# Performance work log

Hardware: AMD Instinct MI355X
Metric: run time of the kernel (lower is better)

Reference implementation:

```python
import jax, jax.numpy as jnp
import numpy as np

D_MODEL = 1024
NUM_HEADS = 16
D_FF = 4096
SEQ = 2048
BATCH = 2
THETA = 10000.0
EPS = 1e-5


def _param(key, shape, fan_in, fan_out):
    std = 2.0 / (fan_in + fan_out) ** 0.5
    return std * jax.random.truncated_normal(key, -3.0, 3.0, shape, dtype=jnp.float32)


def setup_inputs() -> dict:
    key = jax.random.key(0)
    ks = jax.random.split(key, 8)
    d, h, f = D_MODEL, NUM_HEADS, D_FF
    return {
        'x': jax.random.normal(ks[0], (BATCH, SEQ, d), dtype=jnp.float32),
        'token_positions': jnp.arange(SEQ, dtype=jnp.int32),
        'wq': _param(ks[1], (d, d), d, d),
        'wk': _param(ks[2], (d, d), d, d),
        'wv': _param(ks[3], (d, d), d, d),
        'wo': _param(ks[4], (d, d), d, d),
        'ln1_w': jnp.ones((d,), jnp.float32),
        'ln2_w': jnp.ones((d,), jnp.float32),
        'w1': _param(ks[5], (f, d), d, f),
        'w2': _param(ks[6], (d, f), f, d),
        'w3': _param(ks[7], (f, d), d, f),
    }


def rmsnorm(x, w):
    x32 = x.astype(jnp.float32)
    rms = jnp.sqrt(jnp.mean(x32 * x32, axis=-1, keepdims=True) + EPS)
    return ((x32 / rms) * w).astype(x.dtype)


def apply_rope(x, cos, sin):
    # x: [b, h, s, d_k]; cos/sin: [s, d_k//2] -> broadcast as [1,1,s,d_k//2]
    xe, xo = x[..., ::2], x[..., 1::2]
    c = cos[None, None, :, :]
    s = sin[None, None, :, :]
    re = xe * c - xo * s
    ro = xe * s + xo * c
    return jnp.stack((re, ro), axis=-1).reshape(x.shape)


def block_forward(x, token_positions, wq, wk, wv, wo, ln1_w, ln2_w, w1, w2, w3):
    b, s, d = x.shape
    h = NUM_HEADS
    dk = d // h
    # RoPE tables at token positions
    inv_freq = 1.0 / (THETA ** (jnp.arange(0, dk // 2, dtype=jnp.float32) * 2.0 / dk))
    freqs = token_positions.astype(jnp.float32)[:, None] * inv_freq[None, :]  # [s, dk/2]
    cos, sin = jnp.cos(freqs), jnp.sin(freqs)

    # --- attention sublayer (pre-norm) ---
    xn = rmsnorm(x, ln1_w)
    q = jnp.einsum('bsd,ed->bse', xn, wq).reshape(b, s, h, dk).transpose(0, 2, 1, 3)
    k = jnp.einsum('bsd,ed->bse', xn, wk).reshape(b, s, h, dk).transpose(0, 2, 1, 3)
    v = jnp.einsum('bsd,ed->bse', xn, wv).reshape(b, s, h, dk).transpose(0, 2, 1, 3)
    q = apply_rope(q, cos, sin)
    k = apply_rope(k, cos, sin)
    scores = jnp.einsum('bhqd,bhkd->bhqk', q, k) / jnp.sqrt(jnp.float32(dk))
    causal = jnp.tril(jnp.ones((s, s), dtype=bool))
    scores = jnp.where(causal[None, None], scores, -jnp.inf)
    attn = jax.nn.softmax(scores, axis=-1)
    o = jnp.einsum('bhqk,bhkd->bhqd', attn, v)
    o = o.transpose(0, 2, 1, 3).reshape(b, s, d)
    x = x + jnp.einsum('bse,de->bsd', o, wo)

    # --- SwiGLU sublayer (pre-norm) ---
    xn = rmsnorm(x, ln2_w)
    x1 = jnp.einsum('bsd,fd->bsf', xn, w1)
    x3 = jnp.einsum('bsd,fd->bsf', xn, w3)
    gated = (x1 * jax.nn.sigmoid(x1)) * x3
    return x + jnp.einsum('bsf,df->bsd', gated, w2)


def reference(x, token_positions, wq, wk, wv, wo, ln1_w, ln2_w, w1, w2, w3):
    return block_forward(x, token_positions, wq, wk, wv, wo, ln1_w, ln2_w, w1, w2, w3)
```

## Files before the change

### kernel.cpp

```cpp
#include <hip/hip_runtime.h>
#include <hip/hip_bf16.h>

typedef __attribute__((ext_vector_type(4))) float f32x4;
typedef __attribute__((ext_vector_type(8))) short bf16x8;
typedef unsigned short u16;
typedef unsigned int u32;
typedef __attribute__((ext_vector_type(4))) u16 u16x4;

#define DEV static __device__ __forceinline__

constexpr int Bb = 2, Ss = 2048, Dd = 1024, Hh = 16, DKk = 64;
constexpr int Mm = Bb * Ss;

DEV float bf2f(u16 u) { union { u32 i; float f; } v; v.i = (u32)u << 16; return v.f; }
DEV u16 f2bf(float f) {
  union { float f; u32 i; } v; v.f = f;
  u32 r = v.i + 0x7FFFu + ((v.i >> 16) & 1u);
  return (u16)(r >> 16);
}

DEV void gload_lds16(const u16* g, u16* l) {
  __builtin_amdgcn_global_load_lds((const __attribute__((address_space(1))) u32*)g,
                                   (__attribute__((address_space(3))) u32*)l, 16, 0, 0);
}

DEV int swz16(int o) {
  return o ^ (((o >> 8) & 1) << 6) ^ (((o >> 9) & 1) << 5);
}

__global__ void k_cvt_all(const float* __restrict__ wq, const float* __restrict__ wk,
                          const float* __restrict__ wv, const float* __restrict__ wo,
                          const float* __restrict__ w1, const float* __restrict__ w2,
                          const float* __restrict__ w3,
                          u16* __restrict__ wqkv, u16* __restrict__ wob,
                          u16* __restrict__ w13, u16* __restrict__ w2b) {
  int i = (blockIdx.x * 256 + threadIdx.x) * 4;
  int seg = i >> 20;
  const float* src; u16* dst;
  if (seg == 0)      { src = wq + i;             dst = wqkv + i; }
  else if (seg == 1) { src = wk + (i - (1<<20)); dst = wqkv + i; }
  else if (seg == 2) { src = wv + (i - (2<<20)); dst = wqkv + i; }
  else if (seg == 3) { src = wo + (i - (3<<20)); dst = wob  + (i - (3<<20)); }
  else if (seg < 8)  { src = w1 + (i - (4<<20)); dst = w13  + (i - (4<<20)); }
  else if (seg < 12) { src = w2 + (i - (8<<20)); dst = w2b  + (i - (8<<20)); }
  else               { src = w3 + (i - (12<<20)); dst = w13 + (4<<20) + (i - (12<<20)); }
  float4 v = *(const float4*)src;
  u16x4 o = { f2bf(v.x), f2bf(v.y), f2bf(v.z), f2bf(v.w) };
  *(u16x4*)dst = o;
}

__global__ __launch_bounds__(256) void k_rmsnorm(const float* __restrict__ x,
                                                 const float* __restrict__ w,
                                                 u16* __restrict__ out) {
  int row = blockIdx.x;
  int t = threadIdx.x;
  float4 v = ((const float4*)(x + (long)row * Dd))[t];
  float ss = v.x * v.x + v.y * v.y + v.z * v.z + v.w * v.w;
#pragma unroll
  for (int m = 32; m; m >>= 1) ss += __shfl_xor(ss, m, 64);
  __shared__ float red[4];
  if ((t & 63) == 0) red[t >> 6] = ss;
  __syncthreads();
  float tot = red[0] + red[1] + red[2] + red[3];
  float r = rsqrtf(tot * (1.0f / Dd) + 1e-5f);
  float4 wv = ((const float4*)w)[t];
  u16x4 o = { f2bf(v.x * r * wv.x), f2bf(v.y * r * wv.y),
              f2bf(v.z * r * wv.z), f2bf(v.w * r * wv.w) };
  ((u16x4*)(out + (long)row * Dd))[t] = o;
}

__global__ void k_rope(u16* __restrict__ q, u16* __restrict__ k, const int* __restrict__ tp) {
  int idx = blockIdx.x * 256 + threadIdx.x;
  if (idx >= Bb * Ss * Hh * 32) return;
  int p = idx & 31;
  int h = (idx >> 5) & 15;
  int row = idx >> 9;
  int s = row & (Ss - 1);
  float pos = (float)tp[s];
  float invf = __expf(-(float)p * (2.0f / DKk) * 9.2103403719761836f);
  float fr = pos * invf;
  float sn, cs;
  sincosf(fr, &sn, &cs);
  long base = (long)row * Dd + h * DKk + 2 * p;
  float xe = bf2f(q[base]), xo = bf2f(q[base + 1]);
  q[base]     = f2bf((xe * cs - xo * sn) * 0.125f);
  q[base + 1] = f2bf((xe * sn + xo * cs) * 0.125f);
  xe = bf2f(k[base]); xo = bf2f(k[base + 1]);
  k[base]     = f2bf(xe * cs - xo * sn);
  k[base + 1] = f2bf(xe * sn + xo * cs);
}

__global__ void k_gate(u16* __restrict__ x1, const u16* __restrict__ x3, int n) {
  int i = (blockIdx.x * 256 + threadIdx.x) * 4;
  if (i >= n) return;
  u16x4 a = *(u16x4*)(x1 + i);
  u16x4 b = *(const u16x4*)(x3 + i);
#pragma unroll
  for (int j = 0; j < 4; j++) {
    float v = bf2f(a[j]);
    float g = v / (1.0f + __expf(-v)) * bf2f(b[j]);
    a[j] = f2bf(g);
  }
  *(u16x4*)(x1 + i) = a;
}

template <int OM, bool RES>
__global__ __launch_bounds__(256) void k_gemm(const u16* __restrict__ A,
                                              const u16* __restrict__ Bm,
                                              void* __restrict__ Cout,
                                              const float* __restrict__ Rres,
                                              int N, int K) {
  __shared__ u16 Abuf[128 * 32];
  __shared__ u16 Bbuf[128 * 32];
  const int tid = threadIdx.x;
  const int wid = tid >> 6, lane = tid & 63;
  const int wm = wid >> 1, wn = wid & 1;
  const int lq = lane >> 4, ll = lane & 15;
  const int m0 = blockIdx.y * 128, n0 = blockIdx.x * 128;

  f32x4 acc[4][4] = {};

  const int srow = tid >> 2;
  const int scol = (tid & 3) * 8;
  const long aoff = (long)(m0 + srow) * K + scol;
  const long boff = (long)(n0 + srow) * K + scol;
  u16* aldsw = Abuf + wid * 512;
  u16* bldsw = Bbuf + wid * 512;

  for (int k0 = 0; k0 < K; k0 += 32) {
    __syncthreads();
    gload_lds16(A + aoff + k0, aldsw);
    gload_lds16(A + aoff + (long)64 * K + k0, aldsw + 2048);
    gload_lds16(Bm + boff + k0, bldsw);
    gload_lds16(Bm + boff + (long)64 * K + k0, bldsw + 2048);
    __syncthreads();
    bf16x8 af[4], bfr[4];
#pragma unroll
    for (int i = 0; i < 4; i++)
      af[i] = *(const bf16x8*)&Abuf[(wm * 64 + i * 16 + ll) * 32 + lq * 8];
#pragma unroll
    for (int j = 0; j < 4; j++)
      bfr[j] = *(const bf16x8*)&Bbuf[(wn * 64 + j * 16 + ll) * 32 + lq * 8];
#pragma unroll
    for (int i = 0; i < 4; i++)
#pragma unroll
      for (int j = 0; j < 4; j++)
        acc[i][j] = __builtin_amdgcn_mfma_f32_16x16x32_bf16(af[i], bfr[j], acc[i][j], 0, 0, 0);
  }

#pragma unroll
  for (int i = 0; i < 4; i++) {
    const int rowb = m0 + wm * 64 + i * 16 + lq * 4;
#pragma unroll
    for (int j = 0; j < 4; j++) {
      const int col = n0 + wn * 64 + j * 16 + ll;
#pragma unroll
      for (int r = 0; r < 4; r++) {
        int rr = rowb + r;
        float v = acc[i][j][r];
        if (RES) v += Rres[(long)rr * N + col];
        if (OM == 1) {
          ((float*)Cout)[(long)rr * N + col] = v;
        } else {
          ((u16*)Cout)[(long)rr * N + col] = f2bf(v);
        }
      }
    }
  }
}

#define STG_A(d, h, kt)                                                         \
  { gload_lds16(A + aoff[0] + (long)(h) * 128 * K + (kt) * 64, &sA[d][h][dst0]); \
    gload_lds16(A + aoff[1] + (long)(h) * 128 * K + (kt) * 64, &sA[d][h][dst1]); }
#define STG_B(d, h, kt)                                                         \
  { gload_lds16(Bm + boff[0] + (long)(h) * 128 * K + (kt) * 64, &sB[d][h][dst0]); \
    gload_lds16(Bm + boff[1] + (long)(h) * 128 * K + (kt) * 64, &sB[d][h][dst1]); }

#define PHASE(q, d, DOB, WVN, ...)                                              \
  {                                                                             \
    bf16x8 af_[2][2];                                                           \
    _Pragma("unroll") for (int s_ = 0; s_ < 2; s_++)                            \
    _Pragma("unroll") for (int kk_ = 0; kk_ < 2; kk_++) {                       \
      int ms_ = (q) * 4 + wm * 2 + s_;                                          \
      int lo_ = ((ms_ & 7) * 16 + ll) * 128 + kk_ * 64 + lq * 16;               \
      af_[s_][kk_] = *(const bf16x8*)((const char*)sA[d][ms_ >> 3] + swz16(lo_)); \
    }                                                                           \
    if (DOB) {                                                                  \
      _Pragma("unroll") for (int ns_ = 0; ns_ < 4; ns_++)                       \
      _Pragma("unroll") for (int kk_ = 0; kk_ < 2; kk_++) {                     \
        int rl_ = wn * 64 + ns_ * 16 + ll;                                      \
        int lo_ = (rl_ & 127) * 128 + kk_ * 64 + lq * 16;                       \
        bfr[ns_][kk_] = *(const bf16x8*)((const char*)sB[d][rl_ >> 7] + swz16(lo_)); \
      }                                                                         \
    }                                                                           \
    __VA_ARGS__;                                                                \
    __builtin_amdgcn_s_barrier();                                               \
    asm volatile("s_waitcnt lgkmcnt(0)" ::: "memory");                          \
    __builtin_amdgcn_sched_barrier(0);                                          \
    __builtin_amdgcn_s_setprio(1);                                              \
    _Pragma("unroll") for (int s_ = 0; s_ < 2; s_++)                            \
    _Pragma("unroll") for (int ns_ = 0; ns_ < 4; ns_++)                         \
    _Pragma("unroll") for (int kk_ = 0; kk_ < 2; kk_++)                         \
      acc[q][s_][ns_] = __builtin_amdgcn_mfma_f32_16x16x32_bf16(                \
          af_[s_][kk_], bfr[ns_][kk_], acc[q][s_][ns_], 0, 0, 0);               \
    __builtin_amdgcn_s_setprio(0);                                              \
    { int wv_ = (WVN);                                                          \
      if (wv_ == 6) { asm volatile("s_waitcnt vmcnt(6)" ::: "memory"); }        \
      else if (wv_ == 0) { asm volatile("s_waitcnt vmcnt(0)" ::: "memory"); } } \
    __builtin_amdgcn_s_barrier();                                               \
  }

template <int OM>
__global__ __launch_bounds__(512) void k_gemm8(const u16* __restrict__ A,
                                               const u16* __restrict__ Bm,
                                               void* __restrict__ Cout,
                                               int N, int K) {
  __shared__ u16 sA[2][2][8192];
  __shared__ u16 sB[2][2][8192];
  const int nwg = gridDim.x * gridDim.y;
  const int lin = blockIdx.y * gridDim.x + blockIdx.x;
  const int swb = (lin & 7) * (nwg >> 3) + (lin >> 3);
  const int bx = swb % gridDim.x, by = swb / gridDim.x;
  const long m0 = (long)by * 256, n0 = (long)bx * 256;
  const int tid = threadIdx.x;
  const int wid = tid >> 6, lane = tid & 63;
  const int wm = wid >> 2, wn = wid & 3;
  const int lq = lane >> 4, ll = lane & 15;

  long aoff[2], boff[2];
#pragma unroll
  for (int j = 0; j < 2; j++) {
    int off = j * 8192 + wid * 1024 + lane * 16;
    int lo = swz16(off);
    int r = lo >> 7, c = (lo & 127) >> 1;
    aoff[j] = (m0 + r) * K + c;
    boff[j] = (n0 + r) * K + c;
  }
  const int dst0 = wid * 512;
  const int dst1 = 4096 + wid * 512;

  f32x4 acc[4][2][4] = {};
  bf16x8 bfr[4][2];

  const int NT = K >> 6;
  const int NI = NT >> 1;

  STG_A(0, 0, 0); STG_A(0, 1, 0); STG_B(0, 0, 0); STG_B(0, 1, 0);
  STG_B(1, 0, 1); STG_B(1, 1, 1); STG_A(1, 0, 1);
  asm volatile("s_waitcnt vmcnt(6)" ::: "memory");
  __builtin_amdgcn_s_barrier();

  for (int it = 0; it < NI; it++) {
    const int t = 2 * it;
    const bool full = (t + 2 < NT);
    PHASE(0, 0, true,  -1,            STG_A(1, 1, t + 1))
    PHASE(1, 0, false, -1,            if (full) STG_B(0, 0, t + 2))
    PHASE(2, 0, false, -1,            if (full) STG_B(0, 1, t + 2))
    PHASE(3, 0, false, full ? 6 : 0,  if (full) STG_A(0, 0, t + 2))
    PHASE(0, 1, true,  -1,            if (full) STG_A(0, 1, t + 2))
    PHASE(1, 1, false, -1,            if (full) STG_B(1, 0, t + 3))
    PHASE(2, 1, false, -1,            if (full) STG_B(1, 1, t + 3))
    PHASE(3, 1, false, full ? 6 : -1, if (full) STG_A(1, 0, t + 3))
  }

#pragma unroll
  for (int q = 0; q < 4; q++)
#pragma unroll
    for (int s = 0; s < 2; s++) {
      const long row0 = m0 + (q * 4 + wm * 2 + s) * 16 + lq * 4;
#pragma unroll
      for (int ns = 0; ns < 4; ns++) {
        const long col = n0 + wn * 64 + ns * 16 + ll;
#pragma unroll
        for (int r = 0; r < 4; r++) {
          float v = acc[q][s][ns][r];
          long rr = row0 + r;
          if (OM == 3) {
            if (col < 2048) {
              ((u16*)Cout)[(col >> 10) * (long)(Mm * 1024) + rr * 1024 + (col & 1023)] = f2bf(v);
            } else {
              int d = col & 63, hh = ((int)col >> 6) & 15;
              int b2 = (int)rr >> 11, s2 = (int)rr & (Ss - 1);
              ((u16*)Cout)[(long)(2 * Mm * 1024) + ((long)((b2 * Hh + hh) * DKk + d)) * Ss + s2] = f2bf(v);
            }
          } else {
            ((u16*)Cout)[(col >> 12) * ((long)Mm * 4096) + rr * 4096 + (col & 4095)] = f2bf(v);
          }
        }
      }
    }
}

constexpr int PPAD = 80;

DEV void attn_tile(const u16* __restrict__ Kc, const u16* __restrict__ Vc,
                   u16* __restrict__ myP, const bf16x8* qf, f32x4* accO,
                   float* mrow, float* lrow, int qloc, bool diag, int lq, int ll) {
  f32x4 sacc[4] = {};
#pragma unroll
  for (int fn = 0; fn < 4; fn++)
#pragma unroll
    for (int ks = 0; ks < 2; ks++) {
      bf16x8 kf = *(const bf16x8*)&Kc[(fn * 16 + ll) * 64 + (((ks * 4 + lq) ^ (ll & 7)) * 8)];
      sacc[fn] = __builtin_amdgcn_mfma_f32_16x16x32_bf16(qf[ks], kf, sacc[fn], 0, 0, 0);
    }
  float sv[4][4], pmax[4];
#pragma unroll
  for (int r = 0; r < 4; r++) pmax[r] = -1e30f;
#pragma unroll
  for (int fn = 0; fn < 4; fn++) {
    int kc = fn * 16 + ll;
#pragma unroll
    for (int r = 0; r < 4; r++) {
      float v = sacc[fn][r];
      if (diag && kc > qloc + r) v = -1e30f;
      sv[fn][r] = v;
      pmax[r] = fmaxf(pmax[r], v);
    }
  }
#pragma unroll
  for (int r = 0; r < 4; r++) {
#pragma unroll
    for (int m = 1; m < 16; m <<= 1) pmax[r] = fmaxf(pmax[r], __shfl_xor(pmax[r], m, 64));
  }
  float alpha[4], rsum[4];
#pragma unroll
  for (int r = 0; r < 4; r++) {
    float mnew = fmaxf(mrow[r], pmax[r]);
    alpha[r] = __expf(mrow[r] - mnew);
    mrow[r] = mnew;
    rsum[r] = 0.f;
  }
#pragma unroll
  for (int fn = 0; fn < 4; fn++) {
#pragma unroll
    for (int r = 0; r < 4; r++) {
      float p = __expf(sv[fn][r] - mrow[r]);
      rsum[r] += p;
      myP[(lq * 4 + r) * PPAD + fn * 16 + ll] = f2bf(p);
    }
  }
#pragma unroll
  for (int r = 0; r < 4; r++) {
#pragma unroll
    for (int m = 1; m < 16; m <<= 1) rsum[r] += __shfl_xor(rsum[r], m, 64);
    lrow[r] = lrow[r] * alpha[r] + rsum[r];
  }
#pragma unroll
  for (int fn = 0; fn < 4; fn++)
#pragma unroll
    for (int r = 0; r < 4; r++) accO[fn][r] *= alpha[r];
  bf16x8 pa[2];
#pragma unroll
  for (int ks = 0; ks < 2; ks++)
    pa[ks] = *(const bf16x8*)&myP[ll * PPAD + ks * 32 + lq * 8];
#pragma unroll
  for (int fn = 0; fn < 4; fn++)
#pragma unroll
    for (int ks = 0; ks < 2; ks++) {
      bf16x8 vf = *(const bf16x8*)&Vc[(fn * 16 + ll) * 64 + (((ks * 4 + lq) ^ (ll & 7)) * 8)];
      accO[fn] = __builtin_amdgcn_mfma_f32_16x16x32_bf16(pa[ks], vf, accO[fn], 0, 0, 0);
    }
}

__global__ __launch_bounds__(256) void k_attn(const u16* __restrict__ Q,
                                              const u16* __restrict__ Kb,
                                              const u16* __restrict__ VT,
                                              u16* __restrict__ O) {
  __shared__ u16 Kt[2][64 * 64];
  __shared__ u16 Vt[2][64 * 64];
  __shared__ u16 P[4][16 * PPAD];
  const int pair = blockIdx.x;
  const int bh = blockIdx.y;
  const int b = bh >> 4, h = bh & 15;
  const int tid = threadIdx.x;
  const int wid = tid >> 6, lane = tid & 63;
  const int lq = lane >> 4, ll = lane & 15;
  const int qtA = pair, qtB = 31 - pair;
  const int qr0A = qtA * 64 + wid * 16;
  const int qr0B = qtB * 64 + wid * 16;
  const int qloc = wid * 16 + lq * 4;
  const long qkbase = ((long)b * Ss) * Dd + h * DKk;
  const long vbase  = ((long)(b * Hh + h) * DKk) * Ss;
  const int nk = 32 - pair;

  const int slot0 = wid * 64 + lane;
  const int r0 = slot0 >> 3, c0 = (slot0 & 7) ^ (r0 & 7);
  const int slot1 = 256 + slot0;
  const int r1 = slot1 >> 3, c1 = (slot1 & 7) ^ (r1 & 7);
  const int ldsb0 = (wid * 64) * 8;
  const int ldsb1 = (256 + wid * 64) * 8;

  bf16x8 qfA[2], qfB[2];
#pragma unroll
  for (int ks = 0; ks < 2; ks++) {
    qfA[ks] = *(const bf16x8*)&Q[qkbase + (long)(qr0A + ll) * Dd + ks * 32 + lq * 8];
    qfB[ks] = *(const bf16x8*)&Q[qkbase + (long)(qr0B + ll) * Dd + ks * 32 + lq * 8];
  }

  f32x4 accA[4] = {}, accB[4] = {};
  float mA[4], lA[4], mB[4], lB[4];
#pragma unroll
  for (int r = 0; r < 4; r++) { mA[r] = mB[r] = -1e30f; lA[r] = lB[r] = 0.f; }
  u16* myP = P[wid];

  gload_lds16(Kb + qkbase + (long)r0 * Dd + c0 * 8, Kt[0] + ldsb0);
  gload_lds16(Kb + qkbase + (long)r1 * Dd + c1 * 8, Kt[0] + ldsb1);
  gload_lds16(VT + vbase + (long)r0 * Ss + c0 * 8, Vt[0] + ldsb0);
  gload_lds16(VT + vbase + (long)r1 * Ss + c1 * 8, Vt[0] + ldsb1);
  __syncthreads();

  for (int kt = 0; kt < nk; kt++) {
    if (kt + 1 < nk) {
      const int kn = (kt + 1) * 64;
      u16* kd = Kt[(kt + 1) & 1];
      u16* vd = Vt[(kt + 1) & 1];
      gload_lds16(Kb + qkbase + (long)(kn + r0) * Dd + c0 * 8, kd + ldsb0);
      gload_lds16(Kb + qkbase + (long)(kn + r1) * Dd + c1 * 8, kd + ldsb1);
      gload_lds16(VT + vbase + (long)r0 * Ss + kn + c0 * 8, vd + ldsb0);
      gload_lds16(VT + vbase + (long)r1 * Ss + kn + c1 * 8, vd + ldsb1);
    }
    const u16* Kc = Kt[kt & 1];
    const u16* Vc = Vt[kt & 1];

    attn_tile(Kc, Vc, myP, qfB, accB, mB, lB, qloc, kt == nk - 1, lq, ll);
    if (kt <= pair)
      attn_tile(Kc, Vc, myP, qfA, accA, mA, lA, qloc, kt == pair, lq, ll);
    __syncthreads();
  }

#pragma unroll
  for (int fn = 0; fn < 4; fn++) {
#pragma unroll
    for (int r = 0; r < 4; r++) {
      int rowA = qr0A + lq * 4 + r;
      int rowB = qr0B + lq * 4 + r;
      O[((long)(b * Ss + rowA)) * Dd + h * DKk + fn * 16 + ll] = f2bf(accA[fn][r] / lA[r]);
      O[((long)(b * Ss + rowB)) * Dd + h * DKk + fn * 16 + ll] = f2bf(accB[fn][r] / lB[r]);
    }
  }
}

extern "C" void kernel_launch(void* const* d_in, const int* in_sizes, int n_in,
                              void* d_out, int out_size, void* d_ws, size_t ws_size,
                              hipStream_t stream) {
  const float* x   = (const float*)d_in[0];
  const int*   tp  = (const int*)d_in[1];
  const float* wq  = (const float*)d_in[2];
  const float* wk  = (const float*)d_in[3];
  const float* wv  = (const float*)d_in[4];
  const float* wo  = (const float*)d_in[5];
  const float* ln1 = (const float*)d_in[6];
  const float* ln2 = (const float*)d_in[7];
  const float* w1  = (const float*)d_in[8];
  const float* w2  = (const float*)d_in[9];
  const float* w3  = (const float*)d_in[10];

  char* ws = (char*)d_ws;
  const size_t MB = 1024 * 1024;
  u16*   wqkv_b = (u16*)(ws + 0 * MB);
  u16*   wo_b   = (u16*)(ws + 6 * MB);
  u16*   w13_b  = (u16*)(ws + 8 * MB);
  u16*   w2_b   = (u16*)(ws + 24 * MB);
  u16*   xn     = (u16*)(ws + 32 * MB);
  float* x2     = (float*)(ws + 40 * MB);
  u16*   qb     = (u16*)(ws + 56 * MB);
  u16*   kb     = (u16*)(ws + 64 * MB);
  u16*   vtb    = (u16*)(ws + 72 * MB);
  u16*   ob     = (u16*)(ws + 80 * MB);
  u16*   x1     = (u16*)(ws + 56 * MB);
  u16*   x3     = (u16*)(ws + 88 * MB);

  k_cvt_all<<<16384, 256, 0, stream>>>(wq, wk, wv, wo, w1, w2, w3,
                                       wqkv_b, wo_b, w13_b, w2_b);
  k_rmsnorm<<<Mm, 256, 0, stream>>>(x, ln1, xn);
  k_gemm8<3><<<dim3(12, 16), 512, 0, stream>>>(xn, wqkv_b, qb, 3072, 1024);
  k_rope<<<(Bb * Ss * Hh * 32) / 256, 256, 0, stream>>>(qb, kb, tp);
  k_attn<<<dim3(16, 32), 256, 0, stream>>>(qb, kb, vtb, ob);
  k_gemm<1, true><<<dim3(8, 32), 256, 0, stream>>>(ob, wo_b, x2, x, 1024, 1024);
  k_rmsnorm<<<Mm, 256, 0, stream>>>(x2, ln2, xn);
  k_gemm8<4><<<dim3(32, 16), 512, 0, stream>>>(xn, w13_b, x1, 8192, 1024);
  k_gate<<<16384, 256, 0, stream>>>(x1, x3, 4096 * 4096);
  k_gemm<1, true><<<dim3(8, 32), 256, 0, stream>>>(x1, w2_b, (float*)d_out, x2, 1024, 4096);
}
```

Before: 377.8 us.

## Fuse SwiGLU gate into W1/W3 GEMM and retile workgroup-to-block mapping

The W1/W3 GEMM now computes the W1 tile and the W3 tile for the same output block in two passes within one workgroup. It stashes the first result as packed bf16 in registers and applies SiLU gating in the epilogue. This drops the separate gate kernel and the x3 intermediate round trip through HBM. Block-to-tile mapping in both GEMM kernels is changed to grouped chunks (CW x CH per XCD-style group) for better L2 reuse. The cost is higher register pressure from the stash and one extra rounding of x1 to bf16, which matches the previous behaviour.

```diff
diff --git a/kernel.cpp b/kernel.cpp
--- a/kernel.cpp
+++ b/kernel.cpp
@@ -90,20 +90,6 @@
   k[base + 1] = f2bf(xe * sn + xo * cs);
 }
 
-__global__ void k_gate(u16* __restrict__ x1, const u16* __restrict__ x3, int n) {
-  int i = (blockIdx.x * 256 + threadIdx.x) * 4;
-  if (i >= n) return;
-  u16x4 a = *(u16x4*)(x1 + i);
-  u16x4 b = *(const u16x4*)(x3 + i);
-#pragma unroll
-  for (int j = 0; j < 4; j++) {
-    float v = bf2f(a[j]);
-    float g = v / (1.0f + __expf(-v)) * bf2f(b[j]);
-    a[j] = f2bf(g);
-  }
-  *(u16x4*)(x1 + i) = a;
-}
-
 template <int OM, bool RES>
 __global__ __launch_bounds__(256) void k_gemm(const u16* __restrict__ A,
                                               const u16* __restrict__ Bm,
@@ -116,7 +102,12 @@
   const int wid = tid >> 6, lane = tid & 63;
   const int wm = wid >> 1, wn = wid & 1;
   const int lq = lane >> 4, ll = lane & 15;
-  const int m0 = blockIdx.y * 128, n0 = blockIdx.x * 128;
+  const int lin = blockIdx.y * gridDim.x + blockIdx.x;
+  const int c = lin & 7, j = lin >> 3;
+  const int ncc = gridDim.x >> 2;
+  const int bxc = (c % ncc) * 4 + (j & 3);
+  const int byc = (c / ncc) * 8 + (j >> 2);
+  const int m0 = byc * 128, n0 = bxc * 128;
 
   f32x4 acc[4][4] = {};
 
@@ -139,25 +130,25 @@
     for (int i = 0; i < 4; i++)
       af[i] = *(const bf16x8*)&Abuf[(wm * 64 + i * 16 + ll) * 32 + lq * 8];
 #pragma unroll
-    for (int j = 0; j < 4; j++)
-      bfr[j] = *(const bf16x8*)&Bbuf[(wn * 64 + j * 16 + ll) * 32 + lq * 8];
+    for (int j2 = 0; j2 < 4; j2++)
+      bfr[j2] = *(const bf16x8*)&Bbuf[(wn * 64 + j2 * 16 + ll) * 32 + lq * 8];
 #pragma unroll
     for (int i = 0; i < 4; i++)
 #pragma unroll
-      for (int j = 0; j < 4; j++)
-        acc[i][j] = __builtin_amdgcn_mfma_f32_16x16x32_bf16(af[i], bfr[j], acc[i][j], 0, 0, 0);
+      for (int j2 = 0; j2 < 4; j2++)
+        acc[i][j2] = __builtin_amdgcn_mfma_f32_16x16x32_bf16(af[i], bfr[j2], acc[i][j2], 0, 0, 0);
   }
 
 #pragma unroll
   for (int i = 0; i < 4; i++) {
     const int rowb = m0 + wm * 64 + i * 16 + lq * 4;
 #pragma unroll
-    for (int j = 0; j < 4; j++) {
-      const int col = n0 + wn * 64 + j * 16 + ll;
+    for (int j2 = 0; j2 < 4; j2++) {
+      const int col = n0 + wn * 64 + j2 * 16 + ll;
 #pragma unroll
       for (int r = 0; r < 4; r++) {
         int rr = rowb + r;
-        float v = acc[i][j][r];
+        float v = acc[i][j2][r];
         if (RES) v += Rres[(long)rr * N + col];
         if (OM == 1) {
           ((float*)Cout)[(long)rr * N + col] = v;
@@ -173,8 +164,8 @@
   { gload_lds16(A + aoff[0] + (long)(h) * 128 * K + (kt) * 64, &sA[d][h][dst0]); \
     gload_lds16(A + aoff[1] + (long)(h) * 128 * K + (kt) * 64, &sA[d][h][dst1]); }
 #define STG_B(d, h, kt)                                                         \
-  { gload_lds16(Bm + boff[0] + (long)(h) * 128 * K + (kt) * 64, &sB[d][h][dst0]); \
-    gload_lds16(Bm + boff[1] + (long)(h) * 128 * K + (kt) * 64, &sB[d][h][dst1]); }
+  { gload_lds16(Bp + boff[0] + (long)(h) * 128 * K + (kt) * 64, &sB[d][h][dst0]); \
+    gload_lds16(Bp + boff[1] + (long)(h) * 128 * K + (kt) * 64, &sB[d][h][dst1]); }
 
 #define PHASE(q, d, DOB, WVN, ...)                                              \
   {                                                                             \
@@ -210,17 +201,19 @@
     __builtin_amdgcn_s_barrier();                                               \
   }
 
-template <int OM>
+template <int OM, int CW, int CH>
 __global__ __launch_bounds__(512) void k_gemm8(const u16* __restrict__ A,
                                                const u16* __restrict__ Bm,
                                                void* __restrict__ Cout,
                                                int N, int K) {
   __shared__ u16 sA[2][2][8192];
   __shared__ u16 sB[2][2][8192];
-  const int nwg = gridDim.x * gridDim.y;
-  const int lin = blockIdx.y * gridDim.x + blockIdx.x;
-  const int swb = (lin & 7) * (nwg >> 3) + (lin >> 3);
-  const int bx = swb % gridDim.x, by = swb / gridDim.x;
+  const int gx = gridDim.x;
+  const int lin = blockIdx.y * gx + blockIdx.x;
+  const int c = lin & 7, j = lin >> 3;
+  const int ncc = gx / CW;
+  const int bx = (c % ncc) * CW + j % CW;
+  const int by = (c / ncc) * CH + j / CW;
   const long m0 = (long)by * 256, n0 = (long)bx * 256;
   const int tid = threadIdx.x;
   const int wid = tid >> 6, lane = tid & 63;
@@ -229,38 +222,63 @@
 
   long aoff[2], boff[2];
 #pragma unroll
-  for (int j = 0; j < 2; j++) {
-    int off = j * 8192 + wid * 1024 + lane * 16;
+  for (int j2 = 0; j2 < 2; j2++) {
+    int off = j2 * 8192 + wid * 1024 + lane * 16;
     int lo = swz16(off);
-    int r = lo >> 7, c = (lo & 127) >> 1;
-    aoff[j] = (m0 + r) * K + c;
-    boff[j] = (n0 + r) * K + c;
+    int r = lo >> 7, cc = (lo & 127) >> 1;
+    aoff[j2] = (m0 + r) * K + cc;
+    boff[j2] = (n0 + r) * K + cc;
   }
   const int dst0 = wid * 512;
   const int dst1 = 4096 + wid * 512;
 
-  f32x4 acc[4][2][4] = {};
+  f32x4 acc[4][2][4];
   bf16x8 bfr[4][2];
+  u32 stash[4][2][4][2];
 
   const int NT = K >> 6;
   const int NI = NT >> 1;
-
-  STG_A(0, 0, 0); STG_A(0, 1, 0); STG_B(0, 0, 0); STG_B(0, 1, 0);
-  STG_B(1, 0, 1); STG_B(1, 1, 1); STG_A(1, 0, 1);
-  asm volatile("s_waitcnt vmcnt(6)" ::: "memory");
-  __builtin_amdgcn_s_barrier();
-
-  for (int it = 0; it < NI; it++) {
-    const int t = 2 * it;
-    const bool full = (t + 2 < NT);
-    PHASE(0, 0, true,  -1,            STG_A(1, 1, t + 1))
-    PHASE(1, 0, false, -1,            if (full) STG_B(0, 0, t + 2))
-    PHASE(2, 0, false, -1,            if (full) STG_B(0, 1, t + 2))
-    PHASE(3, 0, false, full ? 6 : 0,  if (full) STG_A(0, 0, t + 2))
-    PHASE(0, 1, true,  -1,            if (full) STG_A(0, 1, t + 2))
-    PHASE(1, 1, false, -1,            if (full) STG_B(1, 0, t + 3))
-    PHASE(2, 1, false, -1,            if (full) STG_B(1, 1, t + 3))
-    PHASE(3, 1, false, full ? 6 : -1, if (full) STG_A(1, 0, t + 3))
+  constexpr int REPS = (OM == 5) ? 2 : 1;
+
+  for (int rep = 0; rep < REPS; rep++) {
+    const u16* Bp = Bm + (long)rep * 4096 * K;
+    const f32x4 zz = {0.f, 0.f, 0.f, 0.f};
+#pragma unroll
+    for (int q = 0; q < 4; q++)
+#pragma unroll
+      for (int s = 0; s < 2; s++)
+#pragma unroll
+        for (int ns = 0; ns < 4; ns++) acc[q][s][ns] = zz;
+
+    STG_A(0, 0, 0); STG_A(0, 1, 0); STG_B(0, 0, 0); STG_B(0, 1, 0);
+    STG_B(1, 0, 1); STG_B(1, 1, 1); STG_A(1, 0, 1);
+    asm volatile("s_waitcnt vmcnt(6)" ::: "memory");
+    __builtin_amdgcn_s_barrier();
+
+    for (int it = 0; it < NI; it++) {
+      const int t = 2 * it;
+      const bool full = (t + 2 < NT);
+      PHASE(0, 0, true,  -1,            STG_A(1, 1, t + 1))
+      PHASE(1, 0, false, -1,            if (full) STG_B(0, 0, t + 2))
+      PHASE(2, 0, false, -1,            if (full) STG_B(0, 1, t + 2))
+      PHASE(3, 0, false, full ? 6 : 0,  if (full) STG_A(0, 0, t + 2))
+      PHASE(0, 1, true,  -1,            if (full) STG_A(0, 1, t + 2))
+      PHASE(1, 1, false, -1,            if (full) STG_B(1, 0, t + 3))
+      PHASE(2, 1, false, -1,            if (full) STG_B(1, 1, t + 3))
+      PHASE(3, 1, false, full ? 6 : -1, if (full) STG_A(1, 0, t + 3))
+    }
+
+    if (OM == 5 && rep == 0) {
+#pragma unroll
+      for (int q = 0; q < 4; q++)
+#pragma unroll
+        for (int s = 0; s < 2; s++)
+#pragma unroll
+          for (int ns = 0; ns < 4; ns++) {
+            stash[q][s][ns][0] = (u32)f2bf(acc[q][s][ns][0]) | ((u32)f2bf(acc[q][s][ns][1]) << 16);
+            stash[q][s][ns][1] = (u32)f2bf(acc[q][s][ns][2]) | ((u32)f2bf(acc[q][s][ns][3]) << 16);
+          }
+    }
   }
 
 #pragma unroll
@@ -273,9 +291,9 @@
         const long col = n0 + wn * 64 + ns * 16 + ll;
 #pragma unroll
         for (int r = 0; r < 4; r++) {
-          float v = acc[q][s][ns][r];
           long rr = row0 + r;
           if (OM == 3) {
+            float v = acc[q][s][ns][r];
             if (col < 2048) {
               ((u16*)Cout)[(col >> 10) * (long)(Mm * 1024) + rr * 1024 + (col & 1023)] = f2bf(v);
             } else {
@@ -284,7 +302,12 @@
               ((u16*)Cout)[(long)(2 * Mm * 1024) + ((long)((b2 * Hh + hh) * DKk + d)) * Ss + s2] = f2bf(v);
             }
           } else {
-            ((u16*)Cout)[(col >> 12) * ((long)Mm * 4096) + rr * 4096 + (col & 4095)] = f2bf(v);
+            float v3 = acc[q][s][ns][r];
+            u32 st = stash[q][s][ns][r >> 1];
+            u16 bb = (r & 1) ? (u16)(st >> 16) : (u16)(st & 0xffffu);
+            float v1 = bf2f(bb);
+            float g = v1 / (1.0f + __expf(-v1)) * v3;
+            ((u16*)Cout)[rr * 4096 + col] = f2bf(g);
           }
         }
       }
@@ -469,17 +492,15 @@
   u16*   vtb    = (u16*)(ws + 72 * MB);
   u16*   ob     = (u16*)(ws + 80 * MB);
   u16*   x1     = (u16*)(ws + 56 * MB);
-  u16*   x3     = (u16*)(ws + 88 * MB);
 
   k_cvt_all<<<16384, 256, 0, stream>>>(wq, wk, wv, wo, w1, w2, w3,
                                        wqkv_b, wo_b, w13_b, w2_b);
   k_rmsnorm<<<Mm, 256, 0, stream>>>(x, ln1, xn);
-  k_gemm8<3><<<dim3(12, 16), 512, 0, stream>>>(xn, wqkv_b, qb, 3072, 1024);
+  k_gemm8<3, 6, 4><<<dim3(12, 16), 512, 0, stream>>>(xn, wqkv_b, qb, 3072, 1024);
   k_rope<<<(Bb * Ss * Hh * 32) / 256, 256, 0, stream>>>(qb, kb, tp);
   k_attn<<<dim3(16, 32), 256, 0, stream>>>(qb, kb, vtb, ob);
   k_gemm<1, true><<<dim3(8, 32), 256, 0, stream>>>(ob, wo_b, x2, x, 1024, 1024);
   k_rmsnorm<<<Mm, 256, 0, stream>>>(x2, ln2, xn);
-  k_gemm8<4><<<dim3(32, 16), 512, 0, stream>>>(xn, w13_b, x1, 8192, 1024);
-  k_gate<<<16384, 256, 0, stream>>>(x1, x3, 4096 * 4096);
+  k_gemm8<5, 4, 8><<<dim3(16, 16), 512, 0, stream>>>(xn, w13_b, x1, 4096, 1024);
   k_gemm<1, true><<<dim3(8, 32), 256, 0, stream>>>(x1, w2_b, (float*)d_out, x2, 1024, 4096);
 }
```

After: 380.4 us. No clear change (+0.7%).
